# Optimization experiments

Measured on AMD Instinct MI355X. Metric: run time of the kernel, lower is better.

The kernel has to match this reference:

```python
import jax, jax.numpy as jnp
import numpy as np

QLEN, MLEN, BSZ = 1024, 1024, 8
D_MODEL, N_HEAD, D_HEAD = 512, 8, 64
KLEN = QLEN + MLEN
TAU = 1.0


def _rel_shift(x):
    # x: [qlen, klen, bsz, n_head] -- Transformer-XL relative shift
    q, k, b, n = x.shape
    zero_pad = jnp.zeros((q, 1, b, n), dtype=x.dtype)
    x_padded = jnp.concatenate([zero_pad, x], axis=1).reshape(k + 1, q, b, n)
    return x_padded[1:].reshape(q, k, b, n)


def setup_inputs() -> dict:
    key = jax.random.key(0)
    ks = jax.random.split(key, 8)
    w = jax.random.normal(ks[0], (QLEN, BSZ, D_MODEL), dtype=jnp.float32)
    r = jax.random.normal(ks[1], (KLEN, D_MODEL), dtype=jnp.float32)
    r_w_bias = jax.random.normal(ks[2], (N_HEAD, D_HEAD), dtype=jnp.float32) * 0.02
    r_r_bias = jax.random.normal(ks[3], (N_HEAD, D_HEAD), dtype=jnp.float32) * 0.02
    mems = jax.random.normal(ks[4], (MLEN, BSZ, D_MODEL), dtype=jnp.float32)
    W_qkv = jax.random.normal(ks[5], (D_MODEL, 3 * N_HEAD * D_HEAD), dtype=jnp.float32) * 0.02
    W_r = jax.random.normal(ks[6], (D_MODEL, N_HEAD * D_HEAD), dtype=jnp.float32) * 0.02
    W_o = jax.random.normal(ks[7], (N_HEAD * D_HEAD, D_MODEL), dtype=jnp.float32) * 0.02
    # causal mask with memory: query i can attend keys j <= i + MLEN
    i = jnp.arange(QLEN)[:, None]
    j = jnp.arange(KLEN)[None, :]
    attn_mask = (j > i + MLEN)[:, :, None]  # [qlen, klen, 1] bool, True = masked
    return {"w": w, "r": r, "r_w_bias": r_w_bias, "r_r_bias": r_r_bias,
            "mems": mems, "attn_mask": attn_mask,
            "W_qkv": W_qkv, "W_r": W_r, "W_o": W_o}


def reference(w, r, r_w_bias, r_r_bias, mems, attn_mask, W_qkv, W_r, W_o):
    qlen, bsz, d_model = w.shape
    n_head, d_head = r_w_bias.shape
    scale = 1.0 / np.sqrt(d_head).astype(np.float32)

    cat = jnp.concatenate([mems, w], axis=0)          # [klen, bsz, d_model]
    w_heads = cat @ W_qkv                              # [klen, bsz, 3*n*d]
    w_head_q, w_head_k, w_head_v = jnp.split(w_heads, 3, axis=-1)
    klen = w_head_k.shape[0]
    w_head_q = w_head_q[-qlen:].reshape(qlen, bsz, n_head, d_head)
    w_head_k = w_head_k.reshape(klen, bsz, n_head, d_head)
    w_head_v = w_head_v.reshape(klen, bsz, n_head, d_head)
    r_head_k = (r @ W_r).reshape(-1, n_head, d_head)   # [rlen, n, d]

    AC = jnp.einsum('ibnd,jbnd->ijbn', w_head_q + r_w_bias, w_head_k)
    BD = jnp.einsum('ibnd,jnd->ijbn', w_head_q + r_r_bias, r_head_k)
    BD = _rel_shift(BD)

    attn_score = (AC + BD) * scale                     # [q, k, b, n]
    mask4 = attn_mask[:, :, :, None]                   # [q, k, 1, 1]
    attn_score = jnp.where(mask4, -jnp.inf, attn_score)
    attn_prob = jax.nn.softmax(attn_score * TAU, axis=1)

    # attention entropy per head (no-grad in original)
    p_safe = jnp.where(mask4, 1.0, attn_prob)
    temp = -attn_prob * jnp.log(p_safe)
    attn_entropy = jax.lax.stop_gradient(jnp.mean(jnp.sum(temp, axis=1), axis=(0, 1)))  # [n_head]

    attn_vec = jnp.einsum('ijbn,jbnd->ibnd', attn_prob, w_head_v)
    attn_vec = attn_vec.reshape(qlen, bsz, n_head * d_head)
    attn_out = attn_vec @ W_o                          # [q, b, d_model]
    return attn_out, attn_entropy
```

## Files before the change

kernel.cpp:

```cpp
#include <hip/hip_runtime.h>
#include <hip/hip_bf16.h>


#define QLEN 1024
#define MLEN 1024
#define KLEN 2048
#define BSZ 8
#define DMODEL 512
#define NHEAD 8
#define DHEAD 64
#define RPAD 2176
#define QSC  0.18033688011112042f
#define RTHR 11.54f
#define LN2F 0.6931471805599453f

#define B_QW   0u
#define B_QR   8388608u
#define B_K    16777216u
#define B_VT   33554432u
#define B_R    50331648u
#define B_AVB  52559872u
#define B_ENT  60948480u
#define B_WQT  77729792u
#define B_WRT  81399808u
#define B_WOT  81924096u

typedef short bf16x8 __attribute__((ext_vector_type(8)));
typedef float f32x4  __attribute__((ext_vector_type(4)));

#define SWZ(row, byte) ((((row) << 7) + (((((byte) >> 4) ^ ((row) & 7)) << 4)) + ((byte) & 15)))

__device__ __forceinline__ unsigned short f2bf(float f) {
    union { float f; unsigned int u; } v; v.f = f;
    unsigned int r = v.u + 0x7FFFu + ((v.u >> 16) & 1u);
    return (unsigned short)(r >> 16);
}

__global__ __launch_bounds__(256) void tcvt(const float* __restrict__ S,
                                            unsigned short* __restrict__ D,
                                            int R, int C) {
    __shared__ float t[32][33];
    int bx = blockIdx.x * 32;
    int by = blockIdx.y * 32;
    int x = threadIdx.x & 31, y = threadIdx.x >> 5;
    #pragma unroll
    for (int q = 0; q < 4; ++q)
        t[y + q * 8][x] = S[(size_t)(by + y + q * 8) * C + bx + x];
    __syncthreads();
    #pragma unroll
    for (int q = 0; q < 4; ++q)
        D[(size_t)(bx + y + q * 8) * R + by + x] = f2bf(t[x][y + q * 8]);
}

__global__ void zpad_r(unsigned short* __restrict__ Rg) {
    int idx = blockIdx.x * 256 + threadIdx.x;
    int n = idx >> 10, o = idx & 1023;
    uint4 z = make_uint4(0, 0, 0, 0);
    *reinterpret_cast<uint4*>(Rg + ((size_t)n * RPAD + KLEN) * 64 + o * 8) = z;
}

template<int MODE>
__global__ __launch_bounds__(256) void gemm_mfma(const float* __restrict__ Afa,
                                                 const float* __restrict__ Afb,
                                                 const unsigned short* __restrict__ Abf,
                                                 const unsigned short* __restrict__ Bt,
                                                 const float* __restrict__ rwb,
                                                 const float* __restrict__ rrb,
                                                 unsigned short* __restrict__ QW,
                                                 unsigned short* __restrict__ QR,
                                                 unsigned short* __restrict__ Kg,
                                                 unsigned short* __restrict__ VT,
                                                 unsigned short* __restrict__ Rg,
                                                 float* __restrict__ Cout) {
    __shared__ unsigned short Als[128][72];
    __shared__ unsigned short Bls[128][72];
    const int tid = threadIdx.x;
    const int wv = tid >> 6, lane = tid & 63, lg = lane >> 4, lc = lane & 15;
    const int wr = wv >> 1, wc = wv & 1;
    int n0, m0;
    if (MODE == 0) {
        int id = blockIdx.x + 12 * blockIdx.y;
        int xcd = id & 7, u = id >> 3;
        n0 = (u % 12) * 128;
        m0 = (16 * xcd + u / 12) * 128;
    } else if (MODE == 2) {
        int id = blockIdx.x + 4 * blockIdx.y;
        int xcd = id & 7, u = id >> 3;
        n0 = (u % 4) * 128;
        m0 = (8 * xcd + u / 4) * 128;
    } else {
        n0 = blockIdx.x * 128;
        m0 = blockIdx.y * 128;
    }

    const float* Af = nullptr;
    if (MODE == 0) Af = (m0 < 8192) ? (Afa + (size_t)m0 * 512)
                                    : (Afb + (size_t)(m0 - 8192) * 512);
    else if (MODE == 1) Af = Afa + (size_t)m0 * 512;

    f32x4 acc[4][4];
    #pragma unroll
    for (int mi = 0; mi < 4; ++mi)
        #pragma unroll
        for (int ni = 0; ni < 4; ++ni)
            acc[mi][ni] = (f32x4){0.f, 0.f, 0.f, 0.f};

    for (int k0 = 0; k0 < 512; k0 += 64) {
        __syncthreads();
        #pragma unroll
        for (int q = 0; q < 4; ++q) {
            int c = q * 256 + tid;
            int row = c >> 3, off = (c & 7) * 8;
            if (MODE == 0 || MODE == 1) {
                const float* s = Af + (size_t)row * 512 + k0 + off;
                float4 v0 = *reinterpret_cast<const float4*>(s);
                float4 v1 = *reinterpret_cast<const float4*>(s + 4);
                unsigned int u0, u1, u2, u3;
                asm("v_cvt_pk_bf16_f32 %0, %1, %2" : "=v"(u0) : "v"(v0.x), "v"(v0.y));
                asm("v_cvt_pk_bf16_f32 %0, %1, %2" : "=v"(u1) : "v"(v0.z), "v"(v0.w));
                asm("v_cvt_pk_bf16_f32 %0, %1, %2" : "=v"(u2) : "v"(v1.x), "v"(v1.y));
                asm("v_cvt_pk_bf16_f32 %0, %1, %2" : "=v"(u3) : "v"(v1.z), "v"(v1.w));
                uint4 pk = make_uint4(u0, u1, u2, u3);
                *reinterpret_cast<uint4*>(&Als[row][off]) = pk;
            } else {
                *reinterpret_cast<uint4*>(&Als[row][off]) =
                    *reinterpret_cast<const uint4*>(Abf + (size_t)(m0 + row) * 512 + k0 + off);
            }
            *reinterpret_cast<uint4*>(&Bls[row][off]) =
                *reinterpret_cast<const uint4*>(Bt + (size_t)(n0 + row) * 512 + k0 + off);
        }
        __syncthreads();
        #pragma unroll
        for (int kk = 0; kk < 2; ++kk) {
            bf16x8 af[4], bfr[4];
            #pragma unroll
            for (int mi = 0; mi < 4; ++mi)
                af[mi] = *reinterpret_cast<const bf16x8*>(&Als[64 * wr + 16 * mi + lc][32 * kk + lg * 8]);
            #pragma unroll
            for (int ni = 0; ni < 4; ++ni)
                bfr[ni] = *reinterpret_cast<const bf16x8*>(&Bls[64 * wc + 16 * ni + lc][32 * kk + lg * 8]);
            #pragma unroll
            for (int mi = 0; mi < 4; ++mi)
                #pragma unroll
                for (int ni = 0; ni < 4; ++ni)
                    acc[mi][ni] = __builtin_amdgcn_mfma_f32_16x16x32_bf16(af[mi], bfr[ni], acc[mi][ni], 0, 0, 0);
        }
    }

    #pragma unroll
    for (int mi = 0; mi < 4; ++mi) {
        #pragma unroll
        for (int ni = 0; ni < 4; ++ni) {
            const int n = n0 + 64 * wc + 16 * ni + lc;
            float bw = 0.f, br = 0.f;
            int region = 0, hn = 0, d = 0;
            if (MODE == 0) {
                region = n >> 9; int cr = n & 511; hn = cr >> 6; d = cr & 63;
                if (region == 0) { bw = rwb[hn * 64 + d]; br = rrb[hn * 64 + d]; }
            }
            #pragma unroll
            for (int reg = 0; reg < 4; ++reg) {
                const int m = m0 + 64 * wr + 16 * mi + lg * 4 + reg;
                const float val = acc[mi][ni][reg];
                if (MODE == 0) {
                    int t = m >> 3, b = m & 7, bn = b * 8 + hn;
                    if (region == 0) {
                        if (t >= MLEN) {
                            size_t base = ((size_t)bn * QLEN + (t - MLEN)) * 64 + d;
                            QW[base] = f2bf((val + bw) * QSC);
                            QR[base] = f2bf((val + br) * QSC);
                        }
                    } else if (region == 1) {
                        Kg[((size_t)bn * KLEN + t) * 64 + d] = f2bf(val);
                    } else {
                        int jt = t & 63, bb = jt >> 4, ll = jt & 15;
                        int pj = (bb < 2) ? (2 * ll + bb) : (32 + 2 * ll + (bb - 2));
                        VT[((size_t)bn * 64 + d) * KLEN + (t & ~63) + pj] = f2bf(val);
                    }
                } else if (MODE == 1) {
                    Rg[((size_t)(n >> 6) * RPAD + m) * 64 + (n & 63)] = f2bf(val);
                } else {
                    Cout[(size_t)m * 512 + n] = val;
                }
            }
        }
    }
}

__global__ __launch_bounds__(512, 2) void attn_mfma(const unsigned short* __restrict__ QWg,
                                                    const unsigned short* __restrict__ QRg,
                                                    const unsigned short* __restrict__ Kg,
                                                    const unsigned short* __restrict__ VTg,
                                                    const unsigned short* __restrict__ Rg,
                                                    unsigned short* __restrict__ AVB,
                                                    float* __restrict__ ENT) {
    __shared__ __attribute__((aligned(16))) unsigned short Klds[64 * 64];
    __shared__ __attribute__((aligned(16))) unsigned short Rblds[192 * 64];
    __shared__ __attribute__((aligned(16))) unsigned short Vtlds[64 * 64];
    __shared__ __attribute__((aligned(16))) unsigned short Plds[128 * 64];

    const int tid = threadIdx.x;
    const int w = tid >> 6, lane = tid & 63, lg = lane >> 4, lc = lane & 15;
    const int n = blockIdx.x;
    const int b = blockIdx.y & 7;
    const int kq = blockIdx.y >> 3;
    const int iblk = (kq < 4) ? kq : 11 - kq;
    const int i0 = iblk * 128;
    const int bn = b * 8 + n;
    const int srow = tid >> 3;
    const int sch  = tid & 7;

    {
        const unsigned short* qwsrc = QWg + ((size_t)bn * QLEN + i0) * 64;
        const unsigned short* qrsrc = QRg + ((size_t)bn * QLEN + i0) * 64;
        #pragma unroll
        for (int q = 0; q < 2; ++q) {
            int row = srow + q * 64;
            *reinterpret_cast<uint4*>((char*)Rblds + SWZ(row, sch * 16)) =
                *reinterpret_cast<const uint4*>(qwsrc + (size_t)row * 64 + sch * 8);
            *reinterpret_cast<uint4*>((char*)Plds + SWZ(row, sch * 16)) =
                *reinterpret_cast<const uint4*>(qrsrc + (size_t)row * 64 + sch * 8);
        }
    }
    __syncthreads();
    bf16x8 aqw[2], aqr[2];
    #pragma unroll
    for (int k = 0; k < 2; ++k) {
        aqw[k] = *reinterpret_cast<const bf16x8*>((const char*)Rblds + SWZ(16 * w + lc, 64 * k + 16 * lg));
        aqr[k] = *reinterpret_cast<const bf16x8*>((const char*)Plds + SWZ(16 * w + lc, 64 * k + 16 * lg));
    }

    f32x4 Ofr[4];
    #pragma unroll
    for (int t = 0; t < 4; ++t) Ofr[t] = (f32x4){0.f, 0.f, 0.f, 0.f};
    float mreg[4] = {-1e30f, -1e30f, -1e30f, -1e30f};
    float lpart[4] = {0.f, 0.f, 0.f, 0.f};
    float tpart[4] = {0.f, 0.f, 0.f, 0.f};

    const int nj = 2 * iblk + 18;
    const unsigned short* kbase = Kg  + (size_t)bn * KLEN * 64;
    const unsigned short* vbase = VTg + (size_t)bn * 64 * KLEN;
    const unsigned short* rbase = Rg  + (size_t)n * RPAD * 64 + (size_t)(896 - i0) * 64;

    uint4 kr0, vr0, rr0, rr1, rr2;
    kr0 = *reinterpret_cast<const uint4*>(kbase + (size_t)srow * 64 + sch * 8);
    vr0 = *reinterpret_cast<const uint4*>(vbase + (size_t)srow * KLEN + sch * 8);
    rr0 = *reinterpret_cast<const uint4*>(rbase + (size_t)(srow)       * 64 + sch * 8);
    rr1 = *reinterpret_cast<const uint4*>(rbase + (size_t)(srow + 64)  * 64 + sch * 8);
    rr2 = *reinterpret_cast<const uint4*>(rbase + (size_t)(srow + 128) * 64 + sch * 8);

    for (int jt = 0; jt < nj; ++jt) {
        const int j0 = jt * 64;
        __syncthreads();

        *reinterpret_cast<uint4*>((char*)Klds  + SWZ(srow,       sch * 16)) = kr0;
        *reinterpret_cast<uint4*>((char*)Vtlds + SWZ(srow,       sch * 16)) = vr0;
        *reinterpret_cast<uint4*>((char*)Rblds + SWZ(srow,       sch * 16)) = rr0;
        *reinterpret_cast<uint4*>((char*)Rblds + SWZ(srow + 64,  sch * 16)) = rr1;
        *reinterpret_cast<uint4*>((char*)Rblds + SWZ(srow + 128, sch * 16)) = rr2;

        if (jt + 1 < nj) {
            const int j1 = j0 + 64;
            kr0 = *reinterpret_cast<const uint4*>(kbase + (size_t)(j1 + srow) * 64 + sch * 8);
            vr0 = *reinterpret_cast<const uint4*>(vbase + (size_t)srow * KLEN + j1 + sch * 8);
            rr0 = *reinterpret_cast<const uint4*>(rbase + (size_t)(j1 + srow)       * 64 + sch * 8);
            rr1 = *reinterpret_cast<const uint4*>(rbase + (size_t)(j1 + srow + 64)  * 64 + sch * 8);
            rr2 = *reinterpret_cast<const uint4*>(rbase + (size_t)(j1 + srow + 128) * 64 + sch * 8);
        }

        asm volatile("s_waitcnt lgkmcnt(0)" ::: "memory");
        __builtin_amdgcn_sched_barrier(0);
        __builtin_amdgcn_s_barrier();
        asm volatile("" ::: "memory");
        __builtin_amdgcn_sched_barrier(0);

        __builtin_amdgcn_s_setprio(1);
        f32x4 sfr[4];
        #pragma unroll
        for (int bj = 0; bj < 4; ++bj) {
            f32x4 acc = (f32x4){0.f, 0.f, 0.f, 0.f};
            #pragma unroll
            for (int k = 0; k < 2; ++k) {
                bf16x8 bk = *reinterpret_cast<const bf16x8*>((const char*)Klds + SWZ(16 * bj + lc, 64 * k + 16 * lg));
                acc = __builtin_amdgcn_mfma_f32_16x16x32_bf16(aqw[k], bk, acc, 0, 0, 0);
            }
            sfr[bj] = acc;
        }
        f32x4 g[5];
        const int sb = 112 - 16 * w;
        #pragma unroll
        for (int cb = 0; cb < 5; ++cb) {
            g[cb] = (f32x4){0.f, 0.f, 0.f, 0.f};
            #pragma unroll
            for (int k = 0; k < 2; ++k) {
                bf16x8 br = *reinterpret_cast<const bf16x8*>((const char*)Rblds + SWZ(sb + 16 * cb + lc, 64 * k + 16 * lg));
                g[cb] = __builtin_amdgcn_mfma_f32_16x16x32_bf16(aqr[k], br, g[cb], 0, 0, 0);
            }
        }
        __builtin_amdgcn_s_setprio(0);

        #pragma unroll
        for (int reg = 0; reg < 4; ++reg) {
            int r = lg * 4 + reg;
            int srcl = (lane & 48) | ((lc - r + 15) & 15);
            float gg[5];
            #pragma unroll
            for (int cb = 0; cb < 5; ++cb)
                gg[cb] = __shfl(g[cb][reg], srcl, 64);
            #pragma unroll
            for (int bj = 0; bj < 4; ++bj) {
                float gv = (lc <= r) ? gg[bj] : gg[bj + 1];
                sfr[bj][reg] = sfr[bj][reg] + gv;
            }
        }
        if (jt >= nj - 2) {
            #pragma unroll
            for (int bj = 0; bj < 4; ++bj)
                #pragma unroll
                for (int reg = 0; reg < 4; ++reg) {
                    int ii = 16 * w + lg * 4 + reg;
                    int jj = 16 * bj + lc;
                    if (j0 + jj > i0 + ii + MLEN) sfr[bj][reg] = -1e30f;
                }
        }

        float pm[4];
        #pragma unroll
        for (int reg = 0; reg < 4; ++reg)
            pm[reg] = fmaxf(fmaxf(sfr[0][reg], sfr[1][reg]), fmaxf(sfr[2][reg], sfr[3][reg]));
        bool grow = (pm[0] > mreg[0] + RTHR) || (pm[1] > mreg[1] + RTHR) ||
                    (pm[2] > mreg[2] + RTHR) || (pm[3] > mreg[3] + RTHR);
        if (__any(grow)) {
            #pragma unroll
            for (int reg = 0; reg < 4; ++reg) {
                float gmax = pm[reg];
                gmax = fmaxf(gmax, __shfl_xor(gmax, 1));
                gmax = fmaxf(gmax, __shfl_xor(gmax, 2));
                gmax = fmaxf(gmax, __shfl_xor(gmax, 4));
                gmax = fmaxf(gmax, __shfl_xor(gmax, 8));
                float mo = mreg[reg], mn = fmaxf(mo, gmax);
                float fac = exp2f(mo - mn);
                lpart[reg] *= fac; tpart[reg] *= fac; mreg[reg] = mn;
                Ofr[0][reg] *= fac; Ofr[1][reg] *= fac;
                Ofr[2][reg] *= fac; Ofr[3][reg] *= fac;
            }
        }
        #pragma unroll
        for (int reg = 0; reg < 4; ++reg) {
            float mn = mreg[reg];
            int r = lg * 4 + reg;
            float ee[4];
            float le = 0.f, te = 0.f;
            #pragma unroll
            for (int bj = 0; bj < 4; ++bj) {
                ee[bj] = exp2f(sfr[bj][reg] - mn);
                le += ee[bj]; te += ee[bj] * sfr[bj][reg];
            }
            lpart[reg] += le;
            tpart[reg] += te;
            unsigned int p01, p23;
            asm("v_cvt_pk_bf16_f32 %0, %1, %2" : "=v"(p01) : "v"(ee[0]), "v"(ee[1]));
            asm("v_cvt_pk_bf16_f32 %0, %1, %2" : "=v"(p23) : "v"(ee[2]), "v"(ee[3]));
            *reinterpret_cast<unsigned int*>((char*)Plds + SWZ(16 * w + r, 4 * lc))      = p01;
            *reinterpret_cast<unsigned int*>((char*)Plds + SWZ(16 * w + r, 64 + 4 * lc)) = p23;
        }
        asm volatile("s_waitcnt lgkmcnt(0)" ::: "memory");
        __builtin_amdgcn_sched_barrier(0);

        __builtin_amdgcn_s_setprio(1);
        #pragma unroll
        for (int k = 0; k < 2; ++k) {
            bf16x8 ap = *reinterpret_cast<const bf16x8*>((const char*)Plds + SWZ(16 * w + lc, 64 * k + 16 * lg));
            Ofr[0] = __builtin_amdgcn_mfma_f32_16x16x32_bf16(ap,
                *reinterpret_cast<const bf16x8*>((const char*)Vtlds + SWZ( 0 + lc, 64 * k + 16 * lg)), Ofr[0], 0, 0, 0);
            Ofr[1] = __builtin_amdgcn_mfma_f32_16x16x32_bf16(ap,
                *reinterpret_cast<const bf16x8*>((const char*)Vtlds + SWZ(16 + lc, 64 * k + 16 * lg)), Ofr[1], 0, 0, 0);
            Ofr[2] = __builtin_amdgcn_mfma_f32_16x16x32_bf16(ap,
                *reinterpret_cast<const bf16x8*>((const char*)Vtlds + SWZ(32 + lc, 64 * k + 16 * lg)), Ofr[2], 0, 0, 0);
            Ofr[3] = __builtin_amdgcn_mfma_f32_16x16x32_bf16(ap,
                *reinterpret_cast<const bf16x8*>((const char*)Vtlds + SWZ(48 + lc, 64 * k + 16 * lg)), Ofr[3], 0, 0, 0);
        }
        __builtin_amdgcn_s_setprio(0);
    }

    float lred[4], tred[4];
    #pragma unroll
    for (int reg = 0; reg < 4; ++reg) {
        float l = lpart[reg], t = tpart[reg];
        l += __shfl_xor(l, 1); l += __shfl_xor(l, 2); l += __shfl_xor(l, 4); l += __shfl_xor(l, 8);
        t += __shfl_xor(t, 1); t += __shfl_xor(t, 2); t += __shfl_xor(t, 4); t += __shfl_xor(t, 8);
        lred[reg] = l; tred[reg] = t;
    }

    #pragma unroll
    for (int reg = 0; reg < 4; ++reg) {
        int i = i0 + 16 * w + lg * 4 + reg;
        float inv = 1.f / lred[reg];
        unsigned short* dst = AVB + ((size_t)i * BSZ + b) * DMODEL + n * 64 + lc;
        dst[ 0] = f2bf(Ofr[0][reg] * inv);
        dst[16] = f2bf(Ofr[1][reg] * inv);
        dst[32] = f2bf(Ofr[2][reg] * inv);
        dst[48] = f2bf(Ofr[3][reg] * inv);
    }

    float h = 0.f;
    if (lc == 0) {
        #pragma unroll
        for (int reg = 0; reg < 4; ++reg)
            h += mreg[reg] + log2f(lred[reg]) - tred[reg] / lred[reg];
    }
    h += __shfl_xor(h, 1);  h += __shfl_xor(h, 2);  h += __shfl_xor(h, 4);
    h += __shfl_xor(h, 8);  h += __shfl_xor(h, 16); h += __shfl_xor(h, 32);
    __syncthreads();
    float* hred = reinterpret_cast<float*>(Klds);
    if (lane == 0) hred[w] = h;
    __syncthreads();
    if (tid == 0) {
        float s = 0.f;
        #pragma unroll
        for (int q = 0; q < 8; ++q) s += hred[q];
        ENT[bn * 8 + iblk] = s * LN2F;
    }
}

__global__ void reduce_ent(const float* __restrict__ ent, float* __restrict__ out) {
    int n = threadIdx.x;
    if (n < NHEAD) {
        float s = 0.f;
        for (int b = 0; b < BSZ; ++b)
            for (int it = 0; it < 8; ++it)
                s += ent[(b * NHEAD + n) * 8 + it];
        out[(size_t)QLEN * BSZ * DMODEL + n] = s / (float)(QLEN * BSZ);
    }
}

extern "C" void kernel_launch(void* const* d_in, const int* in_sizes, int n_in,
                              void* d_out, int out_size, void* d_ws, size_t ws_size,
                              hipStream_t stream) {
    const float* w    = (const float*)d_in[0];
    const float* r    = (const float*)d_in[1];
    const float* rwb  = (const float*)d_in[2];
    const float* rrb  = (const float*)d_in[3];
    const float* mems = (const float*)d_in[4];
    const float* Wqkv = (const float*)d_in[6];
    const float* Wr   = (const float*)d_in[7];
    const float* Wo   = (const float*)d_in[8];
    float* out = (float*)d_out;
    char*  wsb = (char*)d_ws;

    unsigned short* QW  = (unsigned short*)(wsb + B_QW);
    unsigned short* QR  = (unsigned short*)(wsb + B_QR);
    unsigned short* Kg  = (unsigned short*)(wsb + B_K);
    unsigned short* VT  = (unsigned short*)(wsb + B_VT);
    unsigned short* Rg  = (unsigned short*)(wsb + B_R);
    unsigned short* AVB = (unsigned short*)(wsb + B_AVB);
    float* ENT = (float*)(wsb + B_ENT);
    unsigned short* WQT = (unsigned short*)(wsb + B_WQT);
    unsigned short* WRT = (unsigned short*)(wsb + B_WRT);
    unsigned short* WOT = (unsigned short*)(wsb + B_WOT);

    tcvt<<<dim3(48, 16), 256, 0, stream>>>(Wqkv, WQT, 512, 1536);
    tcvt<<<dim3(16, 16), 256, 0, stream>>>(Wr, WRT, 512, 512);
    tcvt<<<dim3(16, 16), 256, 0, stream>>>(Wo, WOT, 512, 512);
    zpad_r<<<32, 256, 0, stream>>>(Rg);

    gemm_mfma<0><<<dim3(12, 128), 256, 0, stream>>>(mems, w, nullptr, WQT, rwb, rrb,
                                                    QW, QR, Kg, VT, nullptr, nullptr);
    gemm_mfma<1><<<dim3(4, 16), 256, 0, stream>>>(r, nullptr, nullptr, WRT, nullptr, nullptr,
                                                  nullptr, nullptr, nullptr, nullptr, Rg, nullptr);

    attn_mfma<<<dim3(8, 64), 512, 0, stream>>>(QW, QR, Kg, VT, Rg, AVB, ENT);
    reduce_ent<<<1, 64, 0, stream>>>(ENT, out);

    gemm_mfma<2><<<dim3(4, 64), 256, 0, stream>>>(nullptr, nullptr, AVB, WOT, nullptr, nullptr,
                                                  nullptr, nullptr, nullptr, nullptr, nullptr, out);
}
```

Measured before the change: 230.5 us.

## Double-buffer GEMM LDS tiles and merge weight transpose launches

The projection GEMM kernel now stages its A and B tiles into two LDS buffers, loading the next k-slice while MFMAs consume the current one. This cuts one barrier per iteration and lets global loads overlap compute. The three weight transpose/convert launches are merged into one 3D-grid launch whose surplus blocks exit early, saving launch overhead. The cost is double the LDS per block, which may lower occupancy.

```diff
diff --git a/kernel.cpp b/kernel.cpp
--- a/kernel.cpp
+++ b/kernel.cpp
@@ -36,12 +36,20 @@
     return (unsigned short)(r >> 16);
 }
 
-__global__ __launch_bounds__(256) void tcvt(const float* __restrict__ S,
-                                            unsigned short* __restrict__ D,
-                                            int R, int C) {
+__global__ __launch_bounds__(256) void tcvt3(const float* __restrict__ Wqkv,
+                                             const float* __restrict__ Wr,
+                                             const float* __restrict__ Wo,
+                                             unsigned short* __restrict__ WQT,
+                                             unsigned short* __restrict__ WRT,
+                                             unsigned short* __restrict__ WOT) {
+    const float* S; unsigned short* D; int C;
+    if (blockIdx.z == 0)      { S = Wqkv; D = WQT; C = 1536; }
+    else if (blockIdx.z == 1) { S = Wr;   D = WRT; C = 512;  }
+    else                      { S = Wo;   D = WOT; C = 512;  }
+    int bx = blockIdx.x * 32;
+    if (bx >= C) return;
+    int by = blockIdx.y * 32;
     __shared__ float t[32][33];
-    int bx = blockIdx.x * 32;
-    int by = blockIdx.y * 32;
     int x = threadIdx.x & 31, y = threadIdx.x >> 5;
     #pragma unroll
     for (int q = 0; q < 4; ++q)
@@ -49,7 +57,7 @@
     __syncthreads();
     #pragma unroll
     for (int q = 0; q < 4; ++q)
-        D[(size_t)(bx + y + q * 8) * R + by + x] = f2bf(t[x][y + q * 8]);
+        D[(size_t)(bx + y + q * 8) * 512 + by + x] = f2bf(t[x][y + q * 8]);
 }
 
 __global__ void zpad_r(unsigned short* __restrict__ Rg) {
@@ -72,8 +80,8 @@
                                                  unsigned short* __restrict__ VT,
                                                  unsigned short* __restrict__ Rg,
                                                  float* __restrict__ Cout) {
-    __shared__ unsigned short Als[128][72];
-    __shared__ unsigned short Bls[128][72];
+    __shared__ unsigned short Als[2][128][72];
+    __shared__ unsigned short Bls[2][128][72];
     const int tid = threadIdx.x;
     const int wv = tid >> 6, lane = tid & 63, lg = lane >> 4, lc = lane & 15;
     const int wr = wv >> 1, wc = wv & 1;
@@ -98,15 +106,7 @@
                                     : (Afb + (size_t)(m0 - 8192) * 512);
     else if (MODE == 1) Af = Afa + (size_t)m0 * 512;
 
-    f32x4 acc[4][4];
-    #pragma unroll
-    for (int mi = 0; mi < 4; ++mi)
-        #pragma unroll
-        for (int ni = 0; ni < 4; ++ni)
-            acc[mi][ni] = (f32x4){0.f, 0.f, 0.f, 0.f};
-
-    for (int k0 = 0; k0 < 512; k0 += 64) {
-        __syncthreads();
+    auto STAGE = [&](int buf, int k0) {
         #pragma unroll
         for (int q = 0; q < 4; ++q) {
             int c = q * 256 + tid;
@@ -120,31 +120,44 @@
                 asm("v_cvt_pk_bf16_f32 %0, %1, %2" : "=v"(u1) : "v"(v0.z), "v"(v0.w));
                 asm("v_cvt_pk_bf16_f32 %0, %1, %2" : "=v"(u2) : "v"(v1.x), "v"(v1.y));
                 asm("v_cvt_pk_bf16_f32 %0, %1, %2" : "=v"(u3) : "v"(v1.z), "v"(v1.w));
-                uint4 pk = make_uint4(u0, u1, u2, u3);
-                *reinterpret_cast<uint4*>(&Als[row][off]) = pk;
+                *reinterpret_cast<uint4*>(&Als[buf][row][off]) = make_uint4(u0, u1, u2, u3);
             } else {
-                *reinterpret_cast<uint4*>(&Als[row][off]) =
+                *reinterpret_cast<uint4*>(&Als[buf][row][off]) =
                     *reinterpret_cast<const uint4*>(Abf + (size_t)(m0 + row) * 512 + k0 + off);
             }
-            *reinterpret_cast<uint4*>(&Bls[row][off]) =
+            *reinterpret_cast<uint4*>(&Bls[buf][row][off]) =
                 *reinterpret_cast<const uint4*>(Bt + (size_t)(n0 + row) * 512 + k0 + off);
         }
-        __syncthreads();
+    };
+
+    f32x4 acc[4][4];
+    #pragma unroll
+    for (int mi = 0; mi < 4; ++mi)
+        #pragma unroll
+        for (int ni = 0; ni < 4; ++ni)
+            acc[mi][ni] = (f32x4){0.f, 0.f, 0.f, 0.f};
+
+    STAGE(0, 0);
+    __syncthreads();
+    for (int ks = 0; ks < 8; ++ks) {
+        const int cur = ks & 1;
+        if (ks < 7) STAGE(cur ^ 1, (ks + 1) * 64);
         #pragma unroll
         for (int kk = 0; kk < 2; ++kk) {
             bf16x8 af[4], bfr[4];
             #pragma unroll
             for (int mi = 0; mi < 4; ++mi)
-                af[mi] = *reinterpret_cast<const bf16x8*>(&Als[64 * wr + 16 * mi + lc][32 * kk + lg * 8]);
+                af[mi] = *reinterpret_cast<const bf16x8*>(&Als[cur][64 * wr + 16 * mi + lc][32 * kk + lg * 8]);
             #pragma unroll
             for (int ni = 0; ni < 4; ++ni)
-                bfr[ni] = *reinterpret_cast<const bf16x8*>(&Bls[64 * wc + 16 * ni + lc][32 * kk + lg * 8]);
+                bfr[ni] = *reinterpret_cast<const bf16x8*>(&Bls[cur][64 * wc + 16 * ni + lc][32 * kk + lg * 8]);
             #pragma unroll
             for (int mi = 0; mi < 4; ++mi)
                 #pragma unroll
                 for (int ni = 0; ni < 4; ++ni)
                     acc[mi][ni] = __builtin_amdgcn_mfma_f32_16x16x32_bf16(af[mi], bfr[ni], acc[mi][ni], 0, 0, 0);
         }
+        __syncthreads();
     }
 
     #pragma unroll
@@ -459,9 +472,7 @@
     unsigned short* WRT = (unsigned short*)(wsb + B_WRT);
     unsigned short* WOT = (unsigned short*)(wsb + B_WOT);
 
-    tcvt<<<dim3(48, 16), 256, 0, stream>>>(Wqkv, WQT, 512, 1536);
-    tcvt<<<dim3(16, 16), 256, 0, stream>>>(Wr, WRT, 512, 512);
-    tcvt<<<dim3(16, 16), 256, 0, stream>>>(Wo, WOT, 512, 512);
+    tcvt3<<<dim3(48, 16, 3), 256, 0, stream>>>(Wqkv, Wr, Wo, WQT, WRT, WOT);
     zpad_r<<<32, 256, 0, stream>>>(Rg);
 
     gemm_mfma<0><<<dim3(12, 128), 256, 0, stream>>>(mems, w, nullptr, WQT, rwb, rrb,
```

New measurement: 227.5 us. No clear change (-1.3%).
